# Performance work log

Hardware: AMD Instinct MI355X
Metric: run time of the kernel (lower is better)

Reference implementation:

```python
import jax, jax.numpy as jnp
import numpy as np

INPUT_DIM = 80
ENC_DIM = 256
ATTN_DIM = 128
GRU_DIM = 256
B = 32
T_ENC = 800
T_DEC = 400


def setup_inputs() -> dict:
    key = jax.random.key(0)
    ks = jax.random.split(key, 12)
    s = 0.05
    d = {}
    d['enc_feat'] = jax.random.normal(ks[0], (B, T_ENC, ENC_DIM), jnp.float32)
    d['ground_truth'] = jax.random.normal(ks[1], (B, T_DEC, INPUT_DIM), jnp.float32)
    # GRU (PyTorch layout): weight_ih (3*G, in), weight_hh (3*G, G)
    d['W_ih'] = jax.random.normal(ks[2], (3 * GRU_DIM, INPUT_DIM + ENC_DIM), jnp.float32) * s
    d['W_hh'] = jax.random.normal(ks[3], (3 * GRU_DIM, GRU_DIM), jnp.float32) * s
    d['b_ih'] = jax.random.normal(ks[4], (3 * GRU_DIM,), jnp.float32) * s
    d['b_hh'] = jax.random.normal(ks[5], (3 * GRU_DIM,), jnp.float32) * s
    # Additive attention: v^T tanh(W_enc e + W_dec h + b)
    d['W_enc'] = jax.random.normal(ks[6], (ATTN_DIM, ENC_DIM), jnp.float32) * s
    d['W_dec'] = jax.random.normal(ks[7], (ATTN_DIM, GRU_DIM), jnp.float32) * s
    d['b_attn'] = jax.random.normal(ks[8], (ATTN_DIM,), jnp.float32) * s
    d['v_attn'] = jax.random.normal(ks[9], (ATTN_DIM,), jnp.float32) * s
    # output_trans: Linear(gru_dim + enc_feat_dim -> input_dim)
    d['W_out'] = jax.random.normal(ks[10], (INPUT_DIM, GRU_DIM + ENC_DIM), jnp.float32) * s
    d['b_out'] = jax.random.normal(ks[11], (INPUT_DIM,), jnp.float32) * s
    return d


def reference(enc_feat, ground_truth, W_ih, W_hh, b_ih, b_hh,
              W_enc, W_dec, b_attn, v_attn, W_out, b_out):
    # Teacher-forced decode (teacher_force_rate=1.0): max_step = T_dec,
    # input at each step is ground_truth[:, t, :].
    Bsz, T_enc, E = enc_feat.shape
    G = W_hh.shape[1]
    # Encoder projection for additive attention (step-invariant)
    enc_proj = jnp.einsum('bte,ae->bta', enc_feat, W_enc)  # (B, T_enc, attn_dim)

    def step(carry, x_t):
        h, ctx = carry  # h: (B,G), ctx: (B,E)
        inp = jnp.concatenate([x_t, ctx], axis=-1)  # (B, input_dim+E)
        gi = inp @ W_ih.T + b_ih
        gh = h @ W_hh.T + b_hh
        ir, iz, inn = jnp.split(gi, 3, axis=-1)
        hr, hz, hn = jnp.split(gh, 3, axis=-1)
        r = jax.nn.sigmoid(ir + hr)
        z = jax.nn.sigmoid(iz + hz)
        n = jnp.tanh(inn + r * hn)
        h_new = (1.0 - z) * n + z * h  # PyTorch GRU update
        # additive attention over encoder timesteps
        dec_proj = h_new @ W_dec.T + b_attn  # (B, attn_dim)
        scores = jnp.einsum('bta,a->bt', jnp.tanh(enc_proj + dec_proj[:, None, :]), v_attn)
        attn = jax.nn.softmax(scores, axis=-1)  # (B, T_enc)
        ctx_new = jnp.einsum('bt,bte->be', attn, enc_feat)  # (B, E)
        concat = jnp.concatenate([h_new, ctx_new], axis=-1)
        pred = jax.nn.log_softmax(concat @ W_out.T + b_out, axis=-1)
        return (h_new, ctx_new), (pred, attn)

    h0 = jnp.zeros((Bsz, G), enc_feat.dtype)
    c0 = jnp.zeros((Bsz, E), enc_feat.dtype)
    xs = jnp.swapaxes(ground_truth, 0, 1)  # (T_dec, B, input_dim)
    _, (preds, attns) = jax.lax.scan(step, (h0, c0), xs)
    pred_seq = jnp.swapaxes(preds, 0, 1)    # (B, T_dec, input_dim)
    attn_record = jnp.swapaxes(attns, 0, 1)  # (B, T_dec, T_enc)
    return pred_seq, attn_record
```

## Files before the change

### kernel.cpp

```cpp
#include <hip/hip_runtime.h>

#define BB    32
#define TDEC  400
#define TENC  800
#define EDIM  256
#define GDIM  256
#define ADIM  128
#define IDIM  80
#define G3    768
#define NSL   8
#define SLH   32
#define SLT   100
#define FSTR  16
#define EPST  136
#define ETST  102

typedef unsigned short u16;
typedef unsigned int u32;

__device__ __forceinline__ float b2f(u16 u) {
  union { u32 i; float f; } x; x.i = ((u32)u) << 16; return x.f;
}
__device__ __forceinline__ u16 f2b(float f) {
  union { float f; u32 u; } x; x.f = f;
  u32 u = x.u; u += 0x7fffu + ((u >> 16) & 1u);
  return (u16)(u >> 16);
}
__device__ __forceinline__ void ld8(const u16* p, float* w) {
  const uint4 q = *reinterpret_cast<const uint4*>(p);
  union { u32 i; float f; } c;
  c.i = q.x << 16;          w[0] = c.f;
  c.i = q.x & 0xffff0000u;  w[1] = c.f;
  c.i = q.y << 16;          w[2] = c.f;
  c.i = q.y & 0xffff0000u;  w[3] = c.f;
  c.i = q.z << 16;          w[4] = c.f;
  c.i = q.z & 0xffff0000u;  w[5] = c.f;
  c.i = q.w << 16;          w[6] = c.f;
  c.i = q.w & 0xffff0000u;  w[7] = c.f;
}
__device__ __forceinline__ void ldf8(const float* p, float* w) {
  const float4 a = *reinterpret_cast<const float4*>(p);
  const float4 b = *reinterpret_cast<const float4*>(p + 4);
  w[0] = a.x; w[1] = a.y; w[2] = a.z; w[3] = a.w;
  w[4] = b.x; w[5] = b.y; w[6] = b.z; w[7] = b.w;
}
__device__ __forceinline__ float fsigmoid(float x) {
  return __builtin_amdgcn_rcpf(1.f + __expf(-x));
}
__device__ __forceinline__ float ftanh(float x) {
  float e = __expf(2.f * x);
  return 1.f - 2.f * __builtin_amdgcn_rcpf(e + 1.f);
}
__device__ __forceinline__ void ast(float* p, float v) {
  __hip_atomic_store(p, v, __ATOMIC_RELAXED, __HIP_MEMORY_SCOPE_AGENT);
}
__device__ __forceinline__ float ald(const float* p) {
  return __hip_atomic_load(p, __ATOMIC_RELAXED, __HIP_MEMORY_SCOPE_AGENT);
}
__device__ __forceinline__ void aadd(float* p, float v) {
  (void)__hip_atomic_fetch_add(p, v, __ATOMIC_RELAXED, __HIP_MEMORY_SCOPE_AGENT);
}

__global__ __launch_bounds__(256) void k_gix(
    const float* __restrict__ gt, const float* __restrict__ W_ih,
    const float* __restrict__ b_ih, u16* __restrict__ gi_x) {
  __shared__ float sc_x[8][IDIM];
  const int tid = threadIdx.x;
  const int b = blockIdx.x / 50;
  const int t0 = (blockIdx.x % 50) * 8;
  for (int idx = tid; idx < 8 * IDIM; idx += 256) {
    int row = idx / IDIM, col = idx % IDIM;
    sc_x[row][col] = gt[((size_t)b * TDEC + t0 + row) * IDIM + col];
  }
  __syncthreads();
  for (int kk = 0; kk < 3; ++kk) {
    const int g = tid + 256 * kk;
    const float* wrow = W_ih + (size_t)g * 336;
    float acc[8] = {0,0,0,0,0,0,0,0};
    #pragma unroll 2
    for (int k8 = 0; k8 < IDIM / 8; ++k8) {
      float w[8]; ldf8(wrow + (k8 << 3), w);
      #pragma unroll
      for (int tt = 0; tt < 8; ++tt) {
        const float* x = &sc_x[tt][k8 << 3];
        acc[tt] += w[0]*x[0] + w[1]*x[1] + w[2]*x[2] + w[3]*x[3]
                 + w[4]*x[4] + w[5]*x[5] + w[6]*x[6] + w[7]*x[7];
      }
    }
    const float bias = b_ih[g];
    #pragma unroll
    for (int tt = 0; tt < 8; ++tt)
      gi_x[((size_t)b * TDEC + t0 + tt) * G3 + g] = f2b(acc[tt] + bias);
  }
}

__global__ __launch_bounds__(256) void k_encp(
    const float* __restrict__ enc_feat, const float* __restrict__ W_enc,
    u16* __restrict__ encp, u16* __restrict__ enc_bf) {
  __shared__ float sc_x[16][EDIM];
  const int tid = threadIdx.x;
  const int b = blockIdx.x / 50;
  const int te0 = (blockIdx.x % 50) * 16;
  for (int idx = tid; idx < 16 * EDIM; idx += 256) {
    int row = idx >> 8, col = idx & 255;
    sc_x[row][col] = enc_feat[((size_t)b * TENC + te0 + row) * EDIM + col];
  }
  __syncthreads();
  const int a = tid & 127;
  const int tg = tid >> 7;
  const float* wrow = W_enc + (size_t)a * EDIM;
  float acc[8] = {0,0,0,0,0,0,0,0};
  #pragma unroll 4
  for (int k8 = 0; k8 < EDIM / 8; ++k8) {
    float w[8]; ldf8(wrow + (k8 << 3), w);
    #pragma unroll
    for (int tt = 0; tt < 8; ++tt) {
      const float* x = &sc_x[tg * 8 + tt][k8 << 3];
      acc[tt] += w[0]*x[0] + w[1]*x[1] + w[2]*x[2] + w[3]*x[3]
               + w[4]*x[4] + w[5]*x[5] + w[6]*x[6] + w[7]*x[7];
    }
  }
  #pragma unroll
  for (int tt = 0; tt < 8; ++tt)
    encp[((size_t)b * TENC + te0 + tg * 8 + tt) * ADIM + a] = f2b(acc[tt]);
  for (int idx = tid; idx < 16 * EDIM; idx += 256)
    enc_bf[((size_t)b * TENC + te0) * EDIM + idx] = f2b(sc_x[idx >> 8][idx & 255]);
}

__global__ __launch_bounds__(512, 1) void k_decode(
    const float* __restrict__ W_ih, const float* __restrict__ W_hh,
    const float* __restrict__ b_hh, const float* __restrict__ W_dec,
    const float* __restrict__ b_attn, const float* __restrict__ v_attn,
    const u16* __restrict__ gi_x, const u16* __restrict__ encp,
    const u16* __restrict__ enc_bf, float* __restrict__ stash,
    float* __restrict__ Xh, float* __restrict__ Dacc,
    float* __restrict__ Xctxacc, float* __restrict__ Xsumacc,
    int* __restrict__ flagA, int* __restrict__ flagB,
    float* __restrict__ out_attn) {
  extern __shared__ __align__(16) u16 dynlds[];
  u16* encp_lds = dynlds;
  u16* enc_t    = dynlds + SLT * EPST;

  __shared__ u32 sWdp[ADIM * 17];
  __shared__ __align__(16) float sc_h[256];
  __shared__ float sc_ing[4][68];
  __shared__ float sc_inh[4][68];
  __shared__ float sc_dec[ADIM];
  __shared__ float sc_g0[96];
  __shared__ float sc_g1[96];
  __shared__ float sc_w[104];
  __shared__ float sc_v[ADIM];
  __shared__ float sc_ba[ADIM];
  __shared__ float sc_bhh[96];
  __shared__ float sc_gx[96];
  __shared__ float sc_xs[4];

  const int tid = threadIdx.x;
  const int b = blockIdx.x & 31;
  const int j = blockIdx.x >> 5;
  const int lane = tid & 63;
  const int bank = j & 3;

  u32 wctx[32], whh[32];
  #pragma unroll
  for (int i = 0; i < 32; ++i) { wctx[i] = 0u; whh[i] = 0u; }
  if (tid < 384) {
    const int r = tid >> 2, q = tid & 3;
    const int grow = (r >> 5) * 256 + SLH * j + (r & 31);
    const float2* s1 = reinterpret_cast<const float2*>(
        W_ih + (size_t)grow * 336 + 80 + q * 64);
    const float2* s2 = reinterpret_cast<const float2*>(
        W_hh + (size_t)grow * 256 + q * 64);
    #pragma unroll
    for (int i = 0; i < 32; ++i) {
      const float2 v1 = s1[i], v2 = s2[i];
      wctx[i] = (u32)f2b(v1.x) | ((u32)f2b(v1.y) << 16);
      whh[i]  = (u32)f2b(v2.x) | ((u32)f2b(v2.y) << 16);
    }
  }
  for (int idx = tid; idx < ADIM * 16; idx += 512) {
    const int a = idx >> 4, k2 = idx & 15;
    const float2 v = *reinterpret_cast<const float2*>(
        W_dec + (size_t)a * GDIM + SLH * j + 2 * k2);
    sWdp[a * 17 + k2] = (u32)f2b(v.x) | ((u32)f2b(v.y) << 16);
  }
  for (int idx = tid; idx < SLT * ADIM; idx += 512) {
    const int te = idx >> 7, a = idx & 127;
    encp_lds[te * EPST + a] = encp[((size_t)b * TENC + SLT * j + te) * ADIM + a];
  }
  for (int idx = tid; idx < SLT * EDIM; idx += 512) {
    const int te = idx >> 8, e = idx & 255;
    enc_t[e * ETST + te] = enc_bf[((size_t)b * TENC + SLT * j + te) * EDIM + e];
  }
  if (tid < ADIM) { sc_v[tid] = v_attn[tid]; sc_ba[tid] = b_attn[tid]; }
  if (tid < 96) {
    const int grow = (tid >> 5) * 256 + SLH * j + (tid & 31);
    const float bh = b_hh[grow];
    sc_bhh[tid] = bh;
    sc_g1[tid] = bh;
    sc_gx[tid] = b2f(gi_x[((size_t)b * TDEC + 0) * G3 + grow]);
  }
  if (tid < 256) {
    sc_h[tid] = 0.f;
    sc_ing[tid >> 6][tid & 63] = 0.f;
    sc_inh[tid >> 6][tid & 63] = 0.f;
  }
  __syncthreads();

  for (int t = 0; t < TDEC; ++t) {
    const int p = t & 1;
    if (tid < 384) {
      const float* act = &sc_ing[tid & 3][0];
      float acc = 0.f;
      #pragma unroll
      for (int i = 0; i < 32; ++i) {
        union { u32 u; float f; } lo, hi;
        lo.u = wctx[i] << 16; hi.u = wctx[i] & 0xffff0000u;
        acc += lo.f * act[2 * i] + hi.f * act[2 * i + 1];
      }
      acc += __shfl_xor(acc, 1);
      acc += __shfl_xor(acc, 2);
      if ((tid & 3) == 0) sc_g0[tid >> 2] = acc + sc_gx[tid >> 2];
    }
    __syncthreads();
    if (tid < 64) {
      float hval = 0.f;
      if (lane < SLH) {
        const float gr = sc_g0[lane] + sc_g1[lane];
        const float gz = sc_g0[SLH + lane] + sc_g1[SLH + lane];
        const float rr = fsigmoid(gr);
        const float zz = fsigmoid(gz);
        const float nn = ftanh(sc_g0[2 * SLH + lane] + rr * sc_g1[2 * SLH + lane]);
        const float hp = sc_h[SLH * j + lane];
        hval = (1.f - zz) * nn + zz * hp;
        ast(&Xh[b * GDIM + SLH * j + lane], hval);
      }
      float hn[32];
      #pragma unroll
      for (int k = 0; k < 32; ++k) hn[k] = __shfl(hval, k);
      #pragma unroll
      for (int r2 = 0; r2 < 2; ++r2) {
        const int a = lane + 64 * r2;
        const u32* wp = &sWdp[a * 17];
        float acc = 0.f;
        #pragma unroll
        for (int k2 = 0; k2 < 16; ++k2) {
          const u32 w2 = wp[k2];
          union { u32 u; float f; } lo, hi;
          lo.u = w2 << 16; hi.u = w2 & 0xffff0000u;
          acc += lo.f * hn[2 * k2] + hi.f * hn[2 * k2 + 1];
        }
        aadd(&Dacc[((p * BB + b) * 4 + bank) * ADIM + a], acc);
      }
    }
    __syncthreads();
    if (tid == 0)
      __hip_atomic_store(&flagA[(b * NSL + j) * FSTR], t + 1, __ATOMIC_RELAXED,
                         __HIP_MEMORY_SCOPE_AGENT);
    if (tid < NSL) {
      const int* fp = &flagA[(b * NSL + tid) * FSTR];
      while (__hip_atomic_load(fp, __ATOMIC_RELAXED,
                               __HIP_MEMORY_SCOPE_AGENT) < t + 1)
        __builtin_amdgcn_s_sleep(1);
    }
    __syncthreads();
    if (tid < 256) {
      const float hv = ald(&Xh[b * GDIM + tid]);
      sc_h[tid] = hv;
      sc_inh[tid >> 6][tid & 63] = hv;
      if (j == 0) stash[((size_t)b * TDEC + t) * 512 + tid] = hv;
    }
    if (tid < ADIM) {
      float d = sc_ba[tid];
      #pragma unroll
      for (int k = 0; k < 4; ++k)
        d += ald(&Dacc[((p * BB + b) * 4 + k) * ADIM + tid]);
      sc_dec[tid] = d;
    }
    if (tid >= 256 && tid < 384) {
      const int w = j * 128 + (tid - 256);
      ast(&Xctxacc[(((1 - p) * BB + b) * 4 + (w >> 8)) * EDIM + (w & 255)], 0.f);
    } else if (tid >= 384 && tid < 448) {
      const int w = j * 64 + (tid - 384);
      ast(&Dacc[(((1 - p) * BB + b) * 4 + (w >> 7)) * ADIM + (w & 127)], 0.f);
    } else if (tid == 448 && j < 4) {
      ast(&Xsumacc[(((1 - p) * BB + b) * 4 + j) * FSTR], 0.f);
    }
    __syncthreads();
    if (tid < 400) {
      const int te = tid >> 2, q4 = tid & 3;
      const u16* ep = &encp_lds[te * EPST + q4 * 32];
      const float* dp = sc_dec + q4 * 32;
      const float* vp = sc_v + q4 * 32;
      float s = 0.f;
      #pragma unroll
      for (int k8 = 0; k8 < 4; ++k8) {
        float w[8]; ld8(ep + (k8 << 3), w);
        #pragma unroll
        for (int i = 0; i < 8; ++i) {
          const int a = (k8 << 3) + i;
          s += ftanh(w[i] + dp[a]) * vp[a];
        }
      }
      s += __shfl_xor(s, 1);
      s += __shfl_xor(s, 2);
      if (q4 == 0) sc_w[te] = __expf(s);
    } else if (tid >= 448) {
      const int tn = (t + 1 < TDEC) ? t + 1 : t;
      const int gl = tid - 448;
      {
        const int grow = (gl >> 5) * 256 + SLH * j + (gl & 31);
        sc_gx[gl] = b2f(gi_x[((size_t)b * TDEC + tn) * G3 + grow]);
      }
      if (gl < 32) {
        const int g2 = gl + 64;
        const int grow = (g2 >> 5) * 256 + SLH * j + (g2 & 31);
        sc_gx[g2] = b2f(gi_x[((size_t)b * TDEC + tn) * G3 + grow]);
      }
    }
    __syncthreads();
    if (tid < 64) {
      float v = (lane < 50) ? sc_w[lane] + sc_w[lane + 50] : 0.f;
      #pragma unroll
      for (int off = 1; off < 64; off <<= 1) v += __shfl_xor(v, off);
      if (lane == 0) aadd(&Xsumacc[((p * BB + b) * 4 + bank) * FSTR], v);
    }
    if (tid < 256) {
      const u32* et = reinterpret_cast<const u32*>(&enc_t[tid * ETST]);
      float pc = 0.f;
      #pragma unroll
      for (int k2 = 0; k2 < 50; ++k2) {
        const u32 w2 = et[k2];
        union { u32 u; float f; } lo, hi;
        lo.u = w2 << 16; hi.u = w2 & 0xffff0000u;
        pc += sc_w[2 * k2] * lo.f + sc_w[2 * k2 + 1] * hi.f;
      }
      aadd(&Xctxacc[((p * BB + b) * 4 + bank) * EDIM + tid], pc);
    }
    if (tid < 384) {
      const float* act = &sc_inh[tid & 3][0];
      float acc = 0.f;
      #pragma unroll
      for (int i = 0; i < 32; ++i) {
        union { u32 u; float f; } lo, hi;
        lo.u = whh[i] << 16; hi.u = whh[i] & 0xffff0000u;
        acc += lo.f * act[2 * i] + hi.f * act[2 * i + 1];
      }
      acc += __shfl_xor(acc, 1);
      acc += __shfl_xor(acc, 2);
      if ((tid & 3) == 0) sc_g1[tid >> 2] = acc + sc_bhh[tid >> 2];
    }
    __syncthreads();
    if (tid == 0)
      __hip_atomic_store(&flagB[(b * NSL + j) * FSTR], t + 1, __ATOMIC_RELAXED,
                         __HIP_MEMORY_SCOPE_AGENT);
    if (tid < NSL) {
      const int* fp = &flagB[(b * NSL + tid) * FSTR];
      while (__hip_atomic_load(fp, __ATOMIC_RELAXED,
                               __HIP_MEMORY_SCOPE_AGENT) < t + 1)
        __builtin_amdgcn_s_sleep(1);
      if (tid < 4) sc_xs[tid] = ald(&Xsumacc[((p * BB + b) * 4 + tid) * FSTR]);
    }
    __syncthreads();
    {
      const float S = sc_xs[0] + sc_xs[1] + sc_xs[2] + sc_xs[3];
      const float invS = __builtin_amdgcn_rcpf(S);
      if (tid < 256) {
        float c = 0.f;
        #pragma unroll
        for (int k = 0; k < 4; ++k)
          c += ald(&Xctxacc[((p * BB + b) * 4 + k) * EDIM + tid]);
        const float cv = c * invS;
        sc_ing[tid >> 6][tid & 63] = cv;
        if (j == 0) stash[((size_t)b * TDEC + t) * 512 + 256 + tid] = cv;
      }
      if (tid < SLT)
        out_attn[((size_t)b * TDEC + t) * TENC + SLT * j + tid] =
            sc_w[tid] * invS;
    }
    __syncthreads();
  }
}

__global__ __launch_bounds__(256) void k_pred(
    const float* __restrict__ stash, const float* __restrict__ W_out,
    const float* __restrict__ b_out, float* __restrict__ out_pred) {
  __shared__ float sc_s[4][512];
  __shared__ float sc_lp[2][4][IDIM];
  __shared__ float sc_l[4][IDIM];
  __shared__ float sc_lse[4];
  const int tid = threadIdx.x;
  const int b = blockIdx.x / 100;
  const int t0 = (blockIdx.x % 100) * 4;
  for (int idx = tid; idx < 4 * 512; idx += 256)
    sc_s[idx >> 9][idx & 511] = stash[((size_t)b * TDEC + t0) * 512 + idx];
  __syncthreads();
  const int o = tid & 127, kh = tid >> 7;
  if (o < IDIM) {
    const float* wrow = W_out + (size_t)o * 512 + kh * 256;
    float acc[4] = {0,0,0,0};
    #pragma unroll 4
    for (int k8 = 0; k8 < 32; ++k8) {
      float w[8]; ldf8(wrow + (k8 << 3), w);
      #pragma unroll
      for (int tt = 0; tt < 4; ++tt) {
        const float* x = &sc_s[tt][kh * 256 + (k8 << 3)];
        acc[tt] += w[0]*x[0] + w[1]*x[1] + w[2]*x[2] + w[3]*x[3]
                 + w[4]*x[4] + w[5]*x[5] + w[6]*x[6] + w[7]*x[7];
      }
    }
    #pragma unroll
    for (int tt = 0; tt < 4; ++tt) sc_lp[kh][tt][o] = acc[tt];
  }
  __syncthreads();
  if (tid < IDIM) {
    const float bb = b_out[tid];
    #pragma unroll
    for (int tt = 0; tt < 4; ++tt)
      sc_l[tt][tid] = sc_lp[0][tt][tid] + sc_lp[1][tt][tid] + bb;
  }
  __syncthreads();
  {
    const int w = tid >> 6, lane = tid & 63;
    const float a0 = sc_l[w][lane];
    const float a1 = (lane < IDIM - 64) ? sc_l[w][lane + 64] : -1e30f;
    float m = fmaxf(a0, a1);
    #pragma unroll
    for (int off = 1; off < 64; off <<= 1) m = fmaxf(m, __shfl_xor(m, off));
    float e = __expf(a0 - m) + ((lane < IDIM - 64) ? __expf(a1 - m) : 0.f);
    #pragma unroll
    for (int off = 1; off < 64; off <<= 1) e += __shfl_xor(e, off);
    if (lane == 0) sc_lse[w] = m + __logf(e);
  }
  __syncthreads();
  for (int idx = tid; idx < 4 * IDIM; idx += 256) {
    const int tt = idx / IDIM, oo = idx % IDIM;
    out_pred[((size_t)b * TDEC + t0 + tt) * IDIM + oo] =
        sc_l[tt][oo] - sc_lse[tt];
  }
}

extern "C" void kernel_launch(void* const* d_in, const int* in_sizes, int n_in,
                              void* d_out, int out_size, void* d_ws, size_t ws_size,
                              hipStream_t stream) {
  const float* enc_feat = (const float*)d_in[0];
  const float* gt       = (const float*)d_in[1];
  const float* W_ih     = (const float*)d_in[2];
  const float* W_hh     = (const float*)d_in[3];
  const float* b_ih     = (const float*)d_in[4];
  const float* b_hh     = (const float*)d_in[5];
  const float* W_enc    = (const float*)d_in[6];
  const float* W_dec    = (const float*)d_in[7];
  const float* b_attn   = (const float*)d_in[8];
  const float* v_attn   = (const float*)d_in[9];
  const float* W_out    = (const float*)d_in[10];
  const float* b_out    = (const float*)d_in[11];
  float* out_pred = (float*)d_out;
  float* out_attn = out_pred + (size_t)BB * TDEC * IDIM;

  char* ws = (char*)d_ws;
  size_t off = 0;
  u16* gi_x   = (u16*)(ws + off);   off += (size_t)BB * TDEC * G3 * 2;
  u16* encp   = (u16*)(ws + off);   off += (size_t)BB * TENC * ADIM * 2;
  u16* enc_bf = (u16*)(ws + off);   off += (size_t)BB * TENC * EDIM * 2;
  float* stash= (float*)(ws + off); off += (size_t)BB * TDEC * 512 * 4;
  float* Xh   = (float*)(ws + off); off += (size_t)BB * GDIM * 4;
  char* zbase = ws + off;
  int* flagA    = (int*)(ws + off);   off += (size_t)BB * NSL * FSTR * 4;
  int* flagB    = (int*)(ws + off);   off += (size_t)BB * NSL * FSTR * 4;
  float* Dacc   = (float*)(ws + off); off += (size_t)BB * 2 * 4 * ADIM * 4;
  float* Xctxacc= (float*)(ws + off); off += (size_t)BB * 2 * 4 * EDIM * 4;
  float* Xsumacc= (float*)(ws + off); off += (size_t)BB * 2 * 4 * FSTR * 4;
  const size_t zbytes = (size_t)(ws + off - zbase);

  const int DYNB = (SLT * EPST + EDIM * ETST) * 2;
  static bool s_attr = false;
  if (!s_attr) {
    (void)hipFuncSetAttribute(reinterpret_cast<const void*>(k_decode),
                              hipFuncAttributeMaxDynamicSharedMemorySize, DYNB);
    s_attr = true;
  }

  hipMemsetAsync(zbase, 0, zbytes, stream);

  hipLaunchKernelGGL(k_gix, dim3(BB * 50), dim3(256), 0, stream,
                     gt, W_ih, b_ih, gi_x);
  hipLaunchKernelGGL(k_encp, dim3(BB * 50), dim3(256), 0, stream,
                     enc_feat, W_enc, encp, enc_bf);
  hipLaunchKernelGGL(k_decode, dim3(BB * NSL), dim3(512), DYNB, stream,
                     W_ih, W_hh, b_hh, W_dec, b_attn, v_attn,
                     gi_x, encp, enc_bf, stash, Xh, Dacc, Xctxacc, Xsumacc,
                     flagA, flagB, out_attn);
  hipLaunchKernelGGL(k_pred, dim3(BB * 100), dim3(256), 0, stream,
                     stash, W_out, b_out, out_pred);
}
```

Measured before the change: 3.239 ms.

## Replace flag barriers and atomic accumulation with tagged value-flag slots

Each block now writes its partial results (h slice, attention-projection partials, context partials and softmax sums) as 64-bit {value, step-tag} pairs into per-slice slots. Consumers poll the tags and sum the slices themselves. This removes the separate flag barriers, the float atomic adds, the double-buffer zeroing and two __syncthreads per step, which shortens the cross-block critical path of the sequential decode. In exchange consumers poll 8 slots each, so there is more global polling traffic, and correctness depends on 64-bit atomic stores being seen as a single unit.

```diff
diff --git a/kernel.cpp b/kernel.cpp
--- a/kernel.cpp
+++ b/kernel.cpp
@@ -11,12 +11,13 @@
 #define NSL   8
 #define SLH   32
 #define SLT   100
-#define FSTR  16
+#define XCST  257
 #define EPST  136
 #define ETST  102
 
 typedef unsigned short u16;
 typedef unsigned int u32;
+typedef unsigned long long u64;
 
 __device__ __forceinline__ float b2f(u16 u) {
   union { u32 i; float f; } x; x.i = ((u32)u) << 16; return x.f;
@@ -51,14 +52,38 @@
   float e = __expf(2.f * x);
   return 1.f - 2.f * __builtin_amdgcn_rcpf(e + 1.f);
 }
-__device__ __forceinline__ void ast(float* p, float v) {
-  __hip_atomic_store(p, v, __ATOMIC_RELAXED, __HIP_MEMORY_SCOPE_AGENT);
-}
-__device__ __forceinline__ float ald(const float* p) {
-  return __hip_atomic_load(p, __ATOMIC_RELAXED, __HIP_MEMORY_SCOPE_AGENT);
-}
-__device__ __forceinline__ void aadd(float* p, float v) {
-  (void)__hip_atomic_fetch_add(p, v, __ATOMIC_RELAXED, __HIP_MEMORY_SCOPE_AGENT);
+__device__ __forceinline__ void pst(float2* p, float v, u32 tag) {
+  union { u64 u; u32 w[2]; } pk;
+  pk.w[0] = __float_as_uint(v); pk.w[1] = tag;
+  __hip_atomic_store((u64*)p, pk.u, __ATOMIC_RELAXED, __HIP_MEMORY_SCOPE_AGENT);
+}
+__device__ __forceinline__ u64 pld(const float2* p) {
+  return __hip_atomic_load((const u64*)p, __ATOMIC_RELAXED,
+                           __HIP_MEMORY_SCOPE_AGENT);
+}
+__device__ __forceinline__ float poll1(const float2* p, u32 tag) {
+  for (;;) {
+    const u64 x = pld(p);
+    if ((u32)(x >> 32) == tag) return __uint_as_float((u32)x);
+    __builtin_amdgcn_s_sleep(1);
+  }
+}
+__device__ __forceinline__ float gather8(const float2* base, int stride,
+                                         u32 tag, float init) {
+  u64 x[8];
+  for (;;) {
+    bool ok = true;
+    #pragma unroll
+    for (int k = 0; k < 8; ++k) x[k] = pld(base + (size_t)k * stride);
+    #pragma unroll
+    for (int k = 0; k < 8; ++k) ok &= ((u32)(x[k] >> 32) == tag);
+    if (ok) break;
+    __builtin_amdgcn_s_sleep(1);
+  }
+  float s = init;
+  #pragma unroll
+  for (int k = 0; k < 8; ++k) s += __uint_as_float((u32)x[k]);
+  return s;
 }
 
 __global__ __launch_bounds__(256) void k_gix(
@@ -133,10 +158,8 @@
     const float* __restrict__ b_attn, const float* __restrict__ v_attn,
     const u16* __restrict__ gi_x, const u16* __restrict__ encp,
     const u16* __restrict__ enc_bf, float* __restrict__ stash,
-    float* __restrict__ Xh, float* __restrict__ Dacc,
-    float* __restrict__ Xctxacc, float* __restrict__ Xsumacc,
-    int* __restrict__ flagA, int* __restrict__ flagB,
-    float* __restrict__ out_attn) {
+    float2* __restrict__ XhS, float2* __restrict__ DaccS,
+    float2* __restrict__ XctxS, float* __restrict__ out_attn) {
   extern __shared__ __align__(16) u16 dynlds[];
   u16* encp_lds = dynlds;
   u16* enc_t    = dynlds + SLT * EPST;
@@ -153,13 +176,12 @@
   __shared__ float sc_ba[ADIM];
   __shared__ float sc_bhh[96];
   __shared__ float sc_gx[96];
-  __shared__ float sc_xs[4];
+  __shared__ float sc_S;
 
   const int tid = threadIdx.x;
   const int b = blockIdx.x & 31;
   const int j = blockIdx.x >> 5;
   const int lane = tid & 63;
-  const int bank = j & 3;
 
   u32 wctx[32], whh[32];
   #pragma unroll
@@ -205,10 +227,11 @@
     sc_ing[tid >> 6][tid & 63] = 0.f;
     sc_inh[tid >> 6][tid & 63] = 0.f;
   }
+  float hprev = 0.f;
   __syncthreads();
 
   for (int t = 0; t < TDEC; ++t) {
-    const int p = t & 1;
+    const u32 tag = (u32)(t + 1);
     if (tid < 384) {
       const float* act = &sc_ing[tid & 3][0];
       float acc = 0.f;
@@ -231,9 +254,9 @@
         const float rr = fsigmoid(gr);
         const float zz = fsigmoid(gz);
         const float nn = ftanh(sc_g0[2 * SLH + lane] + rr * sc_g1[2 * SLH + lane]);
-        const float hp = sc_h[SLH * j + lane];
-        hval = (1.f - zz) * nn + zz * hp;
-        ast(&Xh[b * GDIM + SLH * j + lane], hval);
+        hval = (1.f - zz) * nn + zz * hprev;
+        hprev = hval;
+        pst(&XhS[b * GDIM + SLH * j + lane], hval, tag);
       }
       float hn[32];
       #pragma unroll
@@ -250,41 +273,16 @@
           lo.u = w2 << 16; hi.u = w2 & 0xffff0000u;
           acc += lo.f * hn[2 * k2] + hi.f * hn[2 * k2 + 1];
         }
-        aadd(&Dacc[((p * BB + b) * 4 + bank) * ADIM + a], acc);
-      }
-    }
-    __syncthreads();
-    if (tid == 0)
-      __hip_atomic_store(&flagA[(b * NSL + j) * FSTR], t + 1, __ATOMIC_RELAXED,
-                         __HIP_MEMORY_SCOPE_AGENT);
-    if (tid < NSL) {
-      const int* fp = &flagA[(b * NSL + tid) * FSTR];
-      while (__hip_atomic_load(fp, __ATOMIC_RELAXED,
-                               __HIP_MEMORY_SCOPE_AGENT) < t + 1)
-        __builtin_amdgcn_s_sleep(1);
-    }
-    __syncthreads();
-    if (tid < 256) {
-      const float hv = ald(&Xh[b * GDIM + tid]);
-      sc_h[tid] = hv;
-      sc_inh[tid >> 6][tid & 63] = hv;
-      if (j == 0) stash[((size_t)b * TDEC + t) * 512 + tid] = hv;
-    }
-    if (tid < ADIM) {
-      float d = sc_ba[tid];
-      #pragma unroll
-      for (int k = 0; k < 4; ++k)
-        d += ald(&Dacc[((p * BB + b) * 4 + k) * ADIM + tid]);
-      sc_dec[tid] = d;
-    }
-    if (tid >= 256 && tid < 384) {
-      const int w = j * 128 + (tid - 256);
-      ast(&Xctxacc[(((1 - p) * BB + b) * 4 + (w >> 8)) * EDIM + (w & 255)], 0.f);
-    } else if (tid >= 384 && tid < 448) {
-      const int w = j * 64 + (tid - 384);
-      ast(&Dacc[(((1 - p) * BB + b) * 4 + (w >> 7)) * ADIM + (w & 127)], 0.f);
-    } else if (tid == 448 && j < 4) {
-      ast(&Xsumacc[(((1 - p) * BB + b) * 4 + j) * FSTR], 0.f);
+        pst(&DaccS[(b * NSL + j) * ADIM + a], acc, tag);
+      }
+    }
+    if (tid < 128) {
+      sc_dec[tid] = gather8(&DaccS[b * NSL * ADIM + tid], ADIM, tag, sc_ba[tid]);
+    } else if (tid < 384) {
+      const int g = tid - 128;
+      const float hv = poll1(&XhS[b * GDIM + g], tag);
+      sc_h[g] = hv;
+      sc_inh[g >> 6][g & 63] = hv;
     }
     __syncthreads();
     if (tid < 400) {
@@ -305,7 +303,12 @@
       s += __shfl_xor(s, 1);
       s += __shfl_xor(s, 2);
       if (q4 == 0) sc_w[te] = __expf(s);
-    } else if (tid >= 448) {
+    } else if (tid < 448) {
+      if (j == 0) {
+        for (int g = tid - 400; g < 256; g += 48)
+          stash[((size_t)b * TDEC + t) * 512 + g] = sc_h[g];
+      }
+    } else {
       const int tn = (t + 1 < TDEC) ? t + 1 : t;
       const int gl = tid - 448;
       {
@@ -319,12 +322,6 @@
       }
     }
     __syncthreads();
-    if (tid < 64) {
-      float v = (lane < 50) ? sc_w[lane] + sc_w[lane + 50] : 0.f;
-      #pragma unroll
-      for (int off = 1; off < 64; off <<= 1) v += __shfl_xor(v, off);
-      if (lane == 0) aadd(&Xsumacc[((p * BB + b) * 4 + bank) * FSTR], v);
-    }
     if (tid < 256) {
       const u32* et = reinterpret_cast<const u32*>(&enc_t[tid * ETST]);
       float pc = 0.f;
@@ -335,7 +332,13 @@
         lo.u = w2 << 16; hi.u = w2 & 0xffff0000u;
         pc += sc_w[2 * k2] * lo.f + sc_w[2 * k2 + 1] * hi.f;
       }
-      aadd(&Xctxacc[((p * BB + b) * 4 + bank) * EDIM + tid], pc);
+      pst(&XctxS[(b * NSL + j) * XCST + tid], pc, tag);
+    }
+    if (tid < 64) {
+      float v = (lane < 50) ? sc_w[lane] + sc_w[lane + 50] : 0.f;
+      #pragma unroll
+      for (int off = 1; off < 64; off <<= 1) v += __shfl_xor(v, off);
+      if (lane == 0) pst(&XctxS[(b * NSL + j) * XCST + 256], v, tag);
     }
     if (tid < 384) {
       const float* act = &sc_inh[tid & 3][0];
@@ -350,27 +353,17 @@
       acc += __shfl_xor(acc, 2);
       if ((tid & 3) == 0) sc_g1[tid >> 2] = acc + sc_bhh[tid >> 2];
     }
-    __syncthreads();
-    if (tid == 0)
-      __hip_atomic_store(&flagB[(b * NSL + j) * FSTR], t + 1, __ATOMIC_RELAXED,
-                         __HIP_MEMORY_SCOPE_AGENT);
-    if (tid < NSL) {
-      const int* fp = &flagB[(b * NSL + tid) * FSTR];
-      while (__hip_atomic_load(fp, __ATOMIC_RELAXED,
-                               __HIP_MEMORY_SCOPE_AGENT) < t + 1)
-        __builtin_amdgcn_s_sleep(1);
-      if (tid < 4) sc_xs[tid] = ald(&Xsumacc[((p * BB + b) * 4 + tid) * FSTR]);
+    float csum = 0.f;
+    if (tid < 256) {
+      csum = gather8(&XctxS[b * NSL * XCST + tid], XCST, tag, 0.f);
+    } else if (tid == 256) {
+      sc_S = gather8(&XctxS[b * NSL * XCST + 256], XCST, tag, 0.f);
     }
     __syncthreads();
     {
-      const float S = sc_xs[0] + sc_xs[1] + sc_xs[2] + sc_xs[3];
-      const float invS = __builtin_amdgcn_rcpf(S);
+      const float invS = __builtin_amdgcn_rcpf(sc_S);
       if (tid < 256) {
-        float c = 0.f;
-        #pragma unroll
-        for (int k = 0; k < 4; ++k)
-          c += ald(&Xctxacc[((p * BB + b) * 4 + k) * EDIM + tid]);
-        const float cv = c * invS;
+        const float cv = csum * invS;
         sc_ing[tid >> 6][tid & 63] = cv;
         if (j == 0) stash[((size_t)b * TDEC + t) * 512 + 256 + tid] = cv;
       }
@@ -464,13 +457,10 @@
   u16* encp   = (u16*)(ws + off);   off += (size_t)BB * TENC * ADIM * 2;
   u16* enc_bf = (u16*)(ws + off);   off += (size_t)BB * TENC * EDIM * 2;
   float* stash= (float*)(ws + off); off += (size_t)BB * TDEC * 512 * 4;
-  float* Xh   = (float*)(ws + off); off += (size_t)BB * GDIM * 4;
   char* zbase = ws + off;
-  int* flagA    = (int*)(ws + off);   off += (size_t)BB * NSL * FSTR * 4;
-  int* flagB    = (int*)(ws + off);   off += (size_t)BB * NSL * FSTR * 4;
-  float* Dacc   = (float*)(ws + off); off += (size_t)BB * 2 * 4 * ADIM * 4;
-  float* Xctxacc= (float*)(ws + off); off += (size_t)BB * 2 * 4 * EDIM * 4;
-  float* Xsumacc= (float*)(ws + off); off += (size_t)BB * 2 * 4 * FSTR * 4;
+  float2* XhS   = (float2*)(ws + off); off += (size_t)BB * GDIM * 8;
+  float2* DaccS = (float2*)(ws + off); off += (size_t)BB * NSL * ADIM * 8;
+  float2* XctxS = (float2*)(ws + off); off += (size_t)BB * NSL * XCST * 8;
   const size_t zbytes = (size_t)(ws + off - zbase);
 
   const int DYNB = (SLT * EPST + EDIM * ETST) * 2;
@@ -489,8 +479,7 @@
                      enc_feat, W_enc, encp, enc_bf);
   hipLaunchKernelGGL(k_decode, dim3(BB * NSL), dim3(512), DYNB, stream,
                      W_ih, W_hh, b_hh, W_dec, b_attn, v_attn,
-                     gi_x, encp, enc_bf, stash, Xh, Dacc, Xctxacc, Xsumacc,
-                     flagA, flagB, out_attn);
+                     gi_x, encp, enc_bf, stash, XhS, DaccS, XctxS, out_attn);
   hipLaunchKernelGGL(k_pred, dim3(BB * 100), dim3(256), 0, stream,
                      stash, W_out, b_out, out_pred);
 }
```

After: 2.831 ms. -12.6%, faster.
